# Kernel tuning notes

Hardware: AMD Instinct MI355X
Metric: run time of the kernel (lower is better)

The kernel has to match this reference:

```python
import jax, jax.numpy as jnp
from jax import lax
import numpy as np

D_MODEL = 1024
D_STATE = 64
D_CONV = 4
EXPAND = 2
HEADDIM = 64
D_INNER = EXPAND * D_MODEL          # 2048
NHEADS = D_INNER // HEADDIM         # 32
CHUNK = 64
CONV_DIM = D_INNER + 2 * D_STATE    # 2176
D_IN_PROJ = 2 * D_INNER + 2 * D_STATE + NHEADS  # 4256
B_SZ = 4
SEQLEN = 2048
EPS = 1e-5


def _silu(x):
    return x * jax.nn.sigmoid(x)


def _segsum(x):
    # x: [..., T]; returns [..., T, T] with [i,j] = sum_{j<k<=i} x[k], -inf above diag
    T = x.shape[-1]
    xe = jnp.broadcast_to(x[..., None], x.shape + (T,))
    strict_lower = jnp.tril(jnp.ones((T, T), bool), -1)
    xe = jnp.where(strict_lower, xe, 0.0)
    s = jnp.cumsum(xe, axis=-2)
    lower = jnp.tril(jnp.ones((T, T), bool), 0)
    return jnp.where(lower, s, -jnp.inf)


def setup_inputs() -> dict:
    key = jax.random.key(0)
    ks = jax.random.split(key, 5)
    u = jax.random.normal(ks[0], (B_SZ, SEQLEN, D_MODEL), jnp.float32)
    W_in = jax.random.normal(ks[1], (D_IN_PROJ, D_MODEL), jnp.float32) * 0.02
    conv_w = jax.random.normal(ks[2], (CONV_DIM, 1, D_CONV), jnp.float32) * 0.2  # depthwise kernel
    conv_b = jnp.zeros((CONV_DIM,), jnp.float32)
    dt_bias = jax.random.uniform(ks[3], (NHEADS,), jnp.float32, -1.0, 1.0)
    A_log = jnp.log(jnp.linspace(1.0, float(NHEADS), NHEADS)).astype(jnp.float32)
    D = jnp.ones((NHEADS,), jnp.float32)
    norm_w = jnp.ones((D_INNER,), jnp.float32)
    W_out = jax.random.normal(ks[4], (D_MODEL, D_INNER), jnp.float32) * 0.02
    return dict(u=u, W_in=W_in, conv_w=conv_w, conv_b=conv_b, dt_bias=dt_bias,
                A_log=A_log, D=D, norm_w=norm_w, W_out=W_out)


def reference(u, W_in, conv_w, conv_b, dt_bias, A_log, D, norm_w, W_out):
    b, s, _ = u.shape
    A = -jnp.exp(A_log)                                   # [H]
    zxbcdt = u @ W_in.T                                   # [b,s,D_IN_PROJ]
    z = zxbcdt[..., :D_INNER]
    xBC = zxbcdt[..., D_INNER:D_INNER + CONV_DIM]
    dt = jax.nn.softplus(zxbcdt[..., D_INNER + CONV_DIM:] + dt_bias)  # [b,s,H]

    # causal depthwise conv1d (left pad d_conv-1 == torch pad-both + slice[:s])
    xc = lax.conv_general_dilated(
        xBC.transpose(0, 2, 1), conv_w, window_strides=(1,),
        padding=[(D_CONV - 1, 0)], feature_group_count=CONV_DIM,
        dimension_numbers=('NCH', 'OIH', 'NCH'))
    xBC = _silu(xc.transpose(0, 2, 1) + conv_b)           # [b,s,CONV_DIM]

    x = xBC[..., :D_INNER].reshape(b, s, NHEADS, HEADDIM)
    Bm = xBC[..., D_INNER:D_INNER + D_STATE]              # [b,s,N]
    Cm = xBC[..., D_INNER + D_STATE:]                     # [b,s,N]

    # SSD chunked scan
    nch = s // CHUNK
    xs = (x * dt[..., None]).reshape(b, nch, CHUNK, NHEADS, HEADDIM)
    Ad = (A * dt).reshape(b, nch, CHUNK, NHEADS)
    Br = Bm.reshape(b, nch, CHUNK, D_STATE)
    Cr = Cm.reshape(b, nch, CHUNK, D_STATE)
    A_ch = Ad.transpose(0, 1, 3, 2)                       # [b,c,h,l]
    A_cum = jnp.cumsum(A_ch, axis=-1)
    L = jnp.exp(_segsum(A_ch))                            # [b,c,h,l,l]
    Y_diag = jnp.einsum('bcln,bcsn,bchls,bcshp->bclhp', Cr, Br, L, xs)
    decay_states = jnp.exp(A_cum[..., -1:] - A_cum)       # [b,c,h,l]
    states = jnp.einsum('bchl,bcln,bclhp->bchpn', decay_states, Br, xs)
    init = jnp.zeros((b, 1, NHEADS, HEADDIM, D_STATE), xs.dtype)
    states = jnp.concatenate([init, states], axis=1)      # [b,c+1,h,p,n]
    total_decay = jnp.pad(A_cum[..., -1].transpose(0, 2, 1), ((0, 0), (0, 0), (1, 0)))
    decay_chunk = jnp.exp(_segsum(total_decay))           # [b,h,c+1,c+1]
    new_states = jnp.einsum('bhzc,bchpn->bzhpn', decay_chunk, states)
    states = new_states[:, :-1]                           # [b,c,h,p,n]
    state_decay_out = jnp.exp(A_cum)
    Y_off = jnp.einsum('bcln,bchpn,bchl->bclhp', Cr, states, state_decay_out)
    y = (Y_diag + Y_off).reshape(b, s, NHEADS, HEADDIM)

    y = y + x * D[:, None]
    y = y.reshape(b, s, D_INNER)
    # gated RMSNorm
    y = y * _silu(z)
    y = y * lax.rsqrt(jnp.mean(y * y, axis=-1, keepdims=True) + EPS) * norm_w
    return y @ W_out.T
```

## Files before the change

### kernel.cpp

```cpp
#include <hip/hip_runtime.h>
#include <hip/hip_bf16.h>

#define BSZ 4
#define SEQ 2048
#define DMODEL 1024
#define DINNER 2048
#define DSTATE 64
#define NH 32
#define HD 64
#define CKL 64
#define NCH 32
#define CONVD 2176
#define DPROJ 4256
#define N1 4224
#define MTOT 8192
#define YSTR 72

typedef __hip_bfloat16 bf16;
typedef __attribute__((ext_vector_type(8))) short short8;
typedef __attribute__((ext_vector_type(4))) short short4_;
typedef __attribute__((ext_vector_type(4))) float f32x4;

__device__ __forceinline__ float sigmoidf_(float x) { return 1.0f / (1.0f + __expf(-x)); }
__device__ __forceinline__ float bits2f(short s) { return __uint_as_float(((unsigned)(unsigned short)s) << 16); }
__device__ __forceinline__ short f2bits(float f) {
    bf16 h = __float2bfloat16(f);
    return *reinterpret_cast<short*>(&h);
}

__device__ __forceinline__ void gl_lds16(const bf16* g, bf16* l) {
    __builtin_amdgcn_global_load_lds((const __attribute__((address_space(1))) void*)g,
                                     (__attribute__((address_space(3))) void*)l, 16, 0, 0);
}

__device__ __forceinline__ void swzx(int& bx, int& by) {
    int nx = gridDim.x;
    int nwg = nx * gridDim.y;
    int Lr = blockIdx.y * nx + blockIdx.x;
    int L = (Lr & 7) * (nwg >> 3) + (Lr >> 3);
    int GSZ = nx * 8;
    int g = L / GSZ, r = L - g * GSZ;
    bx = r % nx;
    by = g * 8 + r / nx;
}

__global__ void k_cvt2(const float* __restrict__ W_in, const float* __restrict__ W_out,
                       const float* __restrict__ nw, bf16* __restrict__ win_b,
                       bf16* __restrict__ wout_b) {
    int g = (blockIdx.x * 256 + threadIdx.x) * 4;
    if (g < N1 * DMODEL) {
        f32x4 f = *(const f32x4*)&W_in[g];
        short4_ o;
#pragma unroll
        for (int j = 0; j < 4; j++) o[j] = f2bits(f[j]);
        *(short4_*)&win_b[g] = o;
    } else if (g < N1 * DMODEL + DMODEL * DINNER) {
        int g2 = g - N1 * DMODEL;
        f32x4 f = *(const f32x4*)&W_out[g2];
        f32x4 w = *(const f32x4*)&nw[g2 & (DINNER - 1)];
        short4_ o;
#pragma unroll
        for (int j = 0; j < 4; j++) o[j] = f2bits(f[j] * w[j]);
        *(short4_*)&wout_b[g2] = o;
    }
}

__global__ __launch_bounds__(256) void k_gemm_bt(const bf16* __restrict__ A, const bf16* __restrict__ W,
                                                 bf16* __restrict__ C, int N, int K, int lda) {
    __shared__ __align__(16) bf16 lA[128 * 64];
    __shared__ __align__(16) bf16 lB[128 * 64];
    const int tid = threadIdx.x;
    const int lane = tid & 63, w = tid >> 6;
    const int wm = w >> 1, wn = w & 1;
    const int lr = lane & 15, lk = lane >> 4;
    int bx, by;
    swzx(bx, by);
    const int m0 = by * 128, n0 = bx * 128;

    f32x4 acc[4][4];
#pragma unroll
    for (int i = 0; i < 4; i++)
#pragma unroll
        for (int j = 0; j < 4; j++) acc[i][j] = (f32x4){0.f, 0.f, 0.f, 0.f};

    const int r = tid >> 3;
    const int cs = ((tid & 7) ^ (r & 7)) * 8;
    const bf16* ga = A + (size_t)(m0 + r) * lda + cs;
    const bf16* gb = W + (size_t)(n0 + r) * K + cs;
    bf16* la0 = lA + tid * 8;
    bf16* lb0 = lB + tid * 8;
    const int sx = (lr & 7);

    for (int kt = 0; kt < K; kt += 64) {
#pragma unroll
        for (int i = 0; i < 4; i++) {
            gl_lds16(ga + kt + (size_t)(32 * i) * lda, la0 + 2048 * i);
            gl_lds16(gb + kt + (size_t)(32 * i) * K, lb0 + 2048 * i);
        }
        __syncthreads();
#pragma unroll
        for (int hh = 0; hh < 2; hh++) {
            const int cb = ((lk + 4 * hh) ^ sx) * 8;
            short8 af[4], bfr[4];
#pragma unroll
            for (int im = 0; im < 4; im++)
                af[im] = *(const short8*)&lA[(wm * 64 + im * 16 + lr) * 64 + cb];
#pragma unroll
            for (int jn = 0; jn < 4; jn++)
                bfr[jn] = *(const short8*)&lB[(wn * 64 + jn * 16 + lr) * 64 + cb];
#pragma unroll
            for (int im = 0; im < 4; im++)
#pragma unroll
                for (int jn = 0; jn < 4; jn++)
                    acc[im][jn] = __builtin_amdgcn_mfma_f32_16x16x32_bf16(af[im], bfr[jn], acc[im][jn], 0, 0, 0);
        }
        __syncthreads();
    }
#pragma unroll
    for (int im = 0; im < 4; im++) {
        int row = m0 + wm * 64 + im * 16 + lk * 4;
#pragma unroll
        for (int jn = 0; jn < 4; jn++) {
            int col = n0 + wn * 64 + jn * 16 + lr;
            bf16* cp = C + (size_t)row * N + col;
#pragma unroll
            for (int rr = 0; rr < 4; rr++) cp[(size_t)rr * N] = __float2bfloat16(acc[im][jn][rr]);
        }
    }
}

__global__ __launch_bounds__(256) void k_gemm2(const bf16* __restrict__ A, const bf16* __restrict__ W,
                                               float* __restrict__ C) {
    __shared__ __align__(16) bf16 lA[128 * 64];
    __shared__ __align__(16) bf16 lB[128 * 64];
    __shared__ float rsrow[128];
    const int tid = threadIdx.x;
    const int lane = tid & 63, w = tid >> 6;
    const int wm = w >> 1, wn = w & 1;
    const int lr = lane & 15, lk = lane >> 4;
    int bx, by;
    swzx(bx, by);
    const int m0 = by * 128, n0 = bx * 128;
    const int K = DINNER, N = DMODEL;

    f32x4 acc[4][4];
#pragma unroll
    for (int i = 0; i < 4; i++)
#pragma unroll
        for (int j = 0; j < 4; j++) acc[i][j] = (f32x4){0.f, 0.f, 0.f, 0.f};
    float ssq[4] = {0.f, 0.f, 0.f, 0.f};

    const int r = tid >> 3;
    const int cs = ((tid & 7) ^ (r & 7)) * 8;
    const bf16* ga = A + (size_t)(m0 + r) * N1 + cs;
    const bf16* gb = W + (size_t)(n0 + r) * K + cs;
    bf16* la0 = lA + tid * 8;
    bf16* lb0 = lB + tid * 8;
    const int sx = (lr & 7);

    for (int kt = 0; kt < K; kt += 64) {
#pragma unroll
        for (int i = 0; i < 4; i++) {
            gl_lds16(ga + kt + (size_t)(32 * i) * N1, la0 + 2048 * i);
            gl_lds16(gb + kt + (size_t)(32 * i) * K, lb0 + 2048 * i);
        }
        __syncthreads();
#pragma unroll
        for (int hh = 0; hh < 2; hh++) {
            const int cb = ((lk + 4 * hh) ^ sx) * 8;
            short8 af[4], bfr[4];
#pragma unroll
            for (int im = 0; im < 4; im++) {
                af[im] = *(const short8*)&lA[(wm * 64 + im * 16 + lr) * 64 + cb];
#pragma unroll
                for (int j = 0; j < 8; j++) { float v = bits2f(af[im][j]); ssq[im] += v * v; }
            }
#pragma unroll
            for (int jn = 0; jn < 4; jn++)
                bfr[jn] = *(const short8*)&lB[(wn * 64 + jn * 16 + lr) * 64 + cb];
#pragma unroll
            for (int im = 0; im < 4; im++)
#pragma unroll
                for (int jn = 0; jn < 4; jn++)
                    acc[im][jn] = __builtin_amdgcn_mfma_f32_16x16x32_bf16(af[im], bfr[jn], acc[im][jn], 0, 0, 0);
        }
        __syncthreads();
    }
#pragma unroll
    for (int im = 0; im < 4; im++) {
        float s = ssq[im];
        s += __shfl_down(s, 32);
        s += __shfl_down(s, 16);
        if (lane < 16) rsrow[wm * 64 + im * 16 + lane] = rsqrtf(s * (1.0f / DINNER) + 1e-5f);
    }
    __syncthreads();
#pragma unroll
    for (int im = 0; im < 4; im++) {
        int rloc = wm * 64 + im * 16 + lk * 4;
        int row = m0 + rloc;
#pragma unroll
        for (int rr = 0; rr < 4; rr++) {
            float s = rsrow[rloc + rr];
#pragma unroll
            for (int jn = 0; jn < 4; jn++) {
                int col = n0 + wn * 64 + jn * 16 + lr;
                C[(size_t)(row + rr) * N + col] = acc[im][jn][rr] * s;
            }
        }
    }
}

__global__ __launch_bounds__(256) void k_prep(const float* __restrict__ u, const float* __restrict__ W_in,
                                              const float* __restrict__ dt_bias,
                                              bf16* __restrict__ u_b, float* __restrict__ dtt) {
    __shared__ __align__(16) float us[8 * DMODEL];
    const int t0 = blockIdx.x * 8;
    const int tid = threadIdx.x;
    const float* ur = u + (size_t)t0 * DMODEL;
    bf16* ub = u_b + (size_t)t0 * DMODEL;
#pragma unroll
    for (int i = 0; i < 8; i++) {
        int idx = (i * 256 + tid) * 4;
        f32x4 v = *(const f32x4*)&ur[idx];
        *(f32x4*)&us[idx] = v;
        short4_ o;
#pragma unroll
        for (int j = 0; j < 4; j++) o[j] = f2bits(v[j]);
        *(short4_*)&ub[idx] = o;
    }
    __syncthreads();
    const int h = tid >> 3, sub = tid & 7;
    const float* wr = W_in + (size_t)(DPROJ - NH + h) * DMODEL;
    float s[8] = {};
    for (int k = sub * 4; k < DMODEL; k += 32) {
        f32x4 w4 = *(const f32x4*)&wr[k];
#pragma unroll
        for (int rr = 0; rr < 8; rr++) {
            const float* up = &us[rr * DMODEL + k];
            s[rr] += up[0] * w4[0] + up[1] * w4[1] + up[2] * w4[2] + up[3] * w4[3];
        }
    }
#pragma unroll
    for (int rr = 0; rr < 8; rr++) {
        s[rr] += __shfl_down(s[rr], 4, 8);
        s[rr] += __shfl_down(s[rr], 2, 8);
        s[rr] += __shfl_down(s[rr], 1, 8);
    }
    if (sub == 0) {
        float bh = dt_bias[h];
#pragma unroll
        for (int rr = 0; rr < 8; rr++) {
            float x = s[rr] + bh;
            dtt[(size_t)h * MTOT + t0 + rr] = (x > 20.f) ? x : log1pf(__expf(x));
        }
    }
}

__global__ void k_conv(const bf16* __restrict__ zx, const float* __restrict__ cw,
                       const float* __restrict__ cb, bf16* __restrict__ xbc) {
    int g = (blockIdx.x * 256 + threadIdx.x) * 4;
    if (g >= MTOT * CONVD) return;
    int c0 = g % CONVD;
    int t = g / CONVD;
    int s = t & (SEQ - 1);
    const short* base = (const short*)(zx + (size_t)t * N1 + DINNER + c0);
    f32x4 w0 = *(const f32x4*)&cw[(c0 + 0) * 4];
    f32x4 w1 = *(const f32x4*)&cw[(c0 + 1) * 4];
    f32x4 w2 = *(const f32x4*)&cw[(c0 + 2) * 4];
    f32x4 w3 = *(const f32x4*)&cw[(c0 + 3) * 4];
    f32x4 a = *(const f32x4*)&cb[c0];
#pragma unroll
    for (int k = 0; k < 4; k++) {
        int st = s - 3 + k;
        if (st >= 0) {
            short4_ v = *(const short4_*)(base + (long)(k - 3) * N1);
            a[0] += bits2f(v[0]) * w0[k];
            a[1] += bits2f(v[1]) * w1[k];
            a[2] += bits2f(v[2]) * w2[k];
            a[3] += bits2f(v[3]) * w3[k];
        }
    }
    short4_ o;
#pragma unroll
    for (int j = 0; j < 4; j++) o[j] = f2bits(a[j] * sigmoidf_(a[j]));
    *(short4_*)&xbc[g] = o;
}

__global__ __launch_bounds__(256) void k_ssd(const bf16* __restrict__ xbc, const float* __restrict__ dtt,
                                             const float* __restrict__ A_log, const float* __restrict__ Dp,
                                             bf16* __restrict__ zx) {
    __shared__ __align__(16) short Ct[2][64 * YSTR];
    __shared__ __align__(16) short Bt[2][64 * YSTR];
    __shared__ __align__(16) short Bn[2][64 * YSTR];
    __shared__ __align__(16) short Xt[2][32 * YSTR];
    __shared__ __align__(16) short Sb[2][32 * YSTR];
    __shared__ __align__(16) short Gs[4 * 16 * YSTR];
    __shared__ __align__(16) float Sf[32 * 68];
    __shared__ __align__(16) float sdt2[2][64], sAc2[2][64], sf2[2][64];
    __shared__ float set2[2];

    const int ph = blockIdx.x, h = blockIdx.y, b = blockIdx.z;
    const int tid = threadIdx.x;
    const int lane = tid & 63, w = tid >> 6;
    const int lr = lane & 15, lk = lane >> 4;
    const float Ah = -__expf(A_log[h]);
    const float Dh = Dp[h];
    const int xcol = h * HD + ph * 32;

    const int lrow = tid >> 2, c0 = (tid & 3) * 16, px = (tid & 3) * 8;
    const int zl = 16 * w + (lane >> 2), zp = (lane & 3) * 8;

    short8 rC0, rC1, rB0, rB1, rX, rZ;
    float rdt;
    auto load_chunk = [&](int cc) {
        int rows0 = b * SEQ + cc * CKL;
        const short* rp = (const short*)(xbc + (size_t)(rows0 + lrow) * CONVD);
        rC0 = *(const short8*)&rp[DINNER + DSTATE + c0];
        rC1 = *(const short8*)&rp[DINNER + DSTATE + c0 + 8];
        rB0 = *(const short8*)&rp[DINNER + c0];
        rB1 = *(const short8*)&rp[DINNER + c0 + 8];
        rX  = *(const short8*)&rp[xcol + px];
        rZ  = *(const short8*)((const short*)zx + (size_t)(rows0 + zl) * N1 + xcol + zp);
        rdt = dtt[(size_t)h * MTOT + rows0 + lane];
    };
    auto scatter = [&](int buf) {
        *(short8*)&Ct[buf][lrow * YSTR + c0] = rC0;
        *(short8*)&Ct[buf][lrow * YSTR + c0 + 8] = rC1;
        *(short8*)&Bt[buf][lrow * YSTR + c0] = rB0;
        *(short8*)&Bt[buf][lrow * YSTR + c0 + 8] = rB1;
#pragma unroll
        for (int j = 0; j < 8; j++) {
            Bn[buf][(c0 + j) * YSTR + lrow] = rB0[j];
            Bn[buf][(c0 + 8 + j) * YSTR + lrow] = rB1[j];
            Xt[buf][(px + j) * YSTR + lrow] = rX[j];
        }
    };
    auto dtscan = [&](int buf) {
        if (tid < 64) {
            float dv = rdt;
            float v = Ah * dv;
#pragma unroll
            for (int d = 1; d < 64; d <<= 1) { float o = __shfl_up(v, d); if (tid >= d) v += o; }
            float tot = __shfl(v, 63);
            sdt2[buf][tid] = dv; sAc2[buf][tid] = v; sf2[buf][tid] = __expf(tot - v) * dv;
            if (tid == 63) set2[buf] = __expf(tot);
        }
    };

    for (int i = tid; i < 32 * 68; i += 256) Sf[i] = 0.f;
    for (int i = tid; i < 32 * YSTR; i += 256) Sb[0][i] = 0;
    load_chunk(0);
    scatter(0);
    dtscan(0);
    __syncthreads();

    for (int c = 0; c < NCH; c++) {
        const int par = c & 1, nb = par ^ 1;
        const int rows0 = b * SEQ + c * CKL;
        float etot = set2[par];
        short8 zcur = rZ;
        if (c + 1 < NCH) load_chunk(c + 1);

        short8 cf0 = *(const short8*)&Ct[par][(16 * w + lr) * YSTR + lk * 8];
        short8 cf1 = *(const short8*)&Ct[par][(16 * w + lr) * YSTR + 32 + lk * 8];
        f32x4 acc[2];
#pragma unroll
        for (int t = 0; t < 2; t++) {
            short8 s0 = *(const short8*)&Sb[par][(16 * t + lr) * YSTR + lk * 8];
            short8 s1 = *(const short8*)&Sb[par][(16 * t + lr) * YSTR + 32 + lk * 8];
            acc[t] = __builtin_amdgcn_mfma_f32_16x16x32_bf16(cf0, s0, (f32x4){0.f, 0.f, 0.f, 0.f}, 0, 0, 0);
            acc[t] = __builtin_amdgcn_mfma_f32_16x16x32_bf16(cf1, s1, acc[t], 0, 0, 0);
        }
        float sAcl[4], el[4];
#pragma unroll
        for (int rr = 0; rr < 4; rr++) { sAcl[rr] = sAc2[par][16 * w + lk * 4 + rr]; el[rr] = __expf(sAcl[rr]); }
#pragma unroll
        for (int t = 0; t < 2; t++)
#pragma unroll
            for (int rr = 0; rr < 4; rr++) acc[t][rr] *= el[rr];
        short* gw = Gs + w * 16 * YSTR;
#pragma unroll
        for (int t = 0; t < 4; t++) {
            short8 b0 = *(const short8*)&Bt[par][(16 * t + lr) * YSTR + lk * 8];
            short8 b1 = *(const short8*)&Bt[par][(16 * t + lr) * YSTR + 32 + lk * 8];
            f32x4 g = __builtin_amdgcn_mfma_f32_16x16x32_bf16(cf0, b0, (f32x4){0.f, 0.f, 0.f, 0.f}, 0, 0, 0);
            g = __builtin_amdgcn_mfma_f32_16x16x32_bf16(cf1, b1, g, 0, 0, 0);
            int s = 16 * t + lr;
            float sAcs = sAc2[par][s], dts = sdt2[par][s];
#pragma unroll
            for (int rr = 0; rr < 4; rr++) {
                int l = 16 * w + lk * 4 + rr;
                float v = (s <= l) ? g[rr] * __expf(sAcl[rr] - sAcs) * dts : 0.f;
                gw[(lk * 4 + rr) * YSTR + s] = f2bits(v);
            }
        }
        short8 gf0 = *(const short8*)&gw[lr * YSTR + lk * 8];
        short8 gf1 = *(const short8*)&gw[lr * YSTR + 32 + lk * 8];
#pragma unroll
        for (int t = 0; t < 2; t++) {
            short8 x0 = *(const short8*)&Xt[par][(16 * t + lr) * YSTR + lk * 8];
            short8 x1 = *(const short8*)&Xt[par][(16 * t + lr) * YSTR + 32 + lk * 8];
            acc[t] = __builtin_amdgcn_mfma_f32_16x16x32_bf16(gf0, x0, acc[t], 0, 0, 0);
            acc[t] = __builtin_amdgcn_mfma_f32_16x16x32_bf16(gf1, x1, acc[t], 0, 0, 0);
        }
        {
            int pw = w & 1, nh2 = w >> 1;
            short8 xt0 = *(const short8*)&Xt[par][(16 * pw + lr) * YSTR + lk * 8];
            short8 xt1 = *(const short8*)&Xt[par][(16 * pw + lr) * YSTR + 32 + lk * 8];
            f32x4 sa0 = *(const f32x4*)&sf2[par][lk * 8];
            f32x4 sa1 = *(const f32x4*)&sf2[par][lk * 8 + 4];
            f32x4 sb0 = *(const f32x4*)&sf2[par][32 + lk * 8];
            f32x4 sb1 = *(const f32x4*)&sf2[par][32 + lk * 8 + 4];
            short8 xd0, xd1;
#pragma unroll
            for (int j = 0; j < 4; j++) {
                xd0[j]     = f2bits(bits2f(xt0[j])     * sa0[j]);
                xd0[4 + j] = f2bits(bits2f(xt0[4 + j]) * sa1[j]);
                xd1[j]     = f2bits(bits2f(xt1[j])     * sb0[j]);
                xd1[4 + j] = f2bits(bits2f(xt1[4 + j]) * sb1[j]);
            }
#pragma unroll
            for (int j = 0; j < 2; j++) {
                int nt = 2 * nh2 + j;
                short8 b0 = *(const short8*)&Bn[par][(16 * nt + lr) * YSTR + lk * 8];
                short8 b1 = *(const short8*)&Bn[par][(16 * nt + lr) * YSTR + 32 + lk * 8];
                f32x4 sacc = __builtin_amdgcn_mfma_f32_16x16x32_bf16(xd0, b0, (f32x4){0.f, 0.f, 0.f, 0.f}, 0, 0, 0);
                sacc = __builtin_amdgcn_mfma_f32_16x16x32_bf16(xd1, b1, sacc, 0, 0, 0);
#pragma unroll
                for (int rr = 0; rr < 4; rr++) {
                    int n = 16 * nt + lr;
                    int p = 16 * pw + lk * 4 + rr;
                    float nv = Sf[p * 68 + n] * etot + sacc[rr];
                    Sf[p * 68 + n] = nv;
                    Sb[nb][p * YSTR + n] = f2bits(nv);
                }
            }
        }
#pragma unroll
        for (int t = 0; t < 2; t++) {
#pragma unroll
            for (int rr = 0; rr < 4; rr++) {
                int p = 16 * t + lr;
                int l = 16 * w + lk * 4 + rr;
                float y = acc[t][rr] + Dh * bits2f(Xt[par][p * YSTR + l]);
                Ct[par][l * YSTR + p] = f2bits(y);
            }
        }
        {
            short8 y8 = *(const short8*)&Ct[par][zl * YSTR + zp];
            short* zpp = (short*)zx + (size_t)(rows0 + zl) * N1 + xcol + zp;
            short8 o;
#pragma unroll
            for (int j = 0; j < 8; j++) {
                float z = bits2f(zcur[j]);
                o[j] = f2bits(bits2f(y8[j]) * (z * sigmoidf_(z)));
            }
            *(short8*)zpp = o;
        }
        if (c + 1 < NCH) {
            scatter(nb);
            dtscan(nb);
        }
        __syncthreads();
    }
}

extern "C" void kernel_launch(void* const* d_in, const int* in_sizes, int n_in,
                              void* d_out, int out_size, void* d_ws, size_t ws_size,
                              hipStream_t stream) {
    const float* u       = (const float*)d_in[0];
    const float* W_in    = (const float*)d_in[1];
    const float* conv_w  = (const float*)d_in[2];
    const float* conv_b  = (const float*)d_in[3];
    const float* dt_bias = (const float*)d_in[4];
    const float* A_log   = (const float*)d_in[5];
    const float* Dp      = (const float*)d_in[6];
    const float* norm_w  = (const float*)d_in[7];
    const float* W_out   = (const float*)d_in[8];
    float* out = (float*)d_out;

    char* ws = (char*)d_ws;
    bf16* zx     = (bf16*)ws;  ws += (size_t)MTOT * N1 * 2;
    bf16* xbc    = (bf16*)ws;  ws += (size_t)MTOT * CONVD * 2;
    bf16* wout_b = (bf16*)ws;  ws += (size_t)DMODEL * DINNER * 2;
    float* dtt   = (float*)ws; ws += (size_t)NH * MTOT * 4;

    bf16* u_b   = (bf16*)d_out;
    bf16* win_b = (bf16*)((char*)d_out + (size_t)MTOT * DMODEL * 2);

    k_prep<<<MTOT / 8, 256, 0, stream>>>(u, W_in, dt_bias, u_b, dtt);
    k_cvt2<<<((N1 * DMODEL + DMODEL * DINNER) / 4 + 255) / 256, 256, 0, stream>>>(
        W_in, W_out, norm_w, win_b, wout_b);

    k_gemm_bt<<<dim3(N1 / 128, MTOT / 128), 256, 0, stream>>>(u_b, win_b, zx, N1, DMODEL, DMODEL);

    k_conv<<<(MTOT * CONVD / 4 + 255) / 256, 256, 0, stream>>>(zx, conv_w, conv_b, xbc);

    k_ssd<<<dim3(2, NH, BSZ), 256, 0, stream>>>(xbc, dtt, A_log, Dp, zx);

    k_gemm2<<<dim3(DMODEL / 128, MTOT / 128), 256, 0, stream>>>(zx, wout_b, out);
}
```

Measured before the change: 393.8 us.

## Rewrite both GEMMs with larger tiles and software-pipelined LDS buffering

Replaces the two 128x128 single-buffered GEMM kernels with 512-thread kernels on larger tiles: 256x192 for the input projection and 256x128 for the output projection. The new kernels double- or triple-buffer LDS and issue global-to-LDS prefetches for later k-tiles while MFMAs run on the current one. They use explicit vmcnt waits, barriers and s_setprio phases to hide memory latency and remove the stall-heavy sync-load-sync loop. In exchange LDS use and register pressure rise, fewer workgroups are launched, and the hand-counted waitcnt scheduling is fragile.

```diff
diff --git a/kernel.cpp b/kernel.cpp
--- a/kernel.cpp
+++ b/kernel.cpp
@@ -33,6 +33,17 @@
                                      (__attribute__((address_space(3))) void*)l, 16, 0, 0);
 }
 
+__device__ __forceinline__ f32x4 MF(short8 a, short8 b, f32x4 c) {
+    return __builtin_amdgcn_mfma_f32_16x16x32_bf16(a, b, c, 0, 0, 0);
+}
+
+template<int N> __device__ __forceinline__ void vmw() {
+    if constexpr (N == 0)      asm volatile("s_waitcnt vmcnt(0)" ::: "memory");
+    else if constexpr (N == 3) asm volatile("s_waitcnt vmcnt(3)" ::: "memory");
+    else if constexpr (N == 6) asm volatile("s_waitcnt vmcnt(6)" ::: "memory");
+    else                       asm volatile("s_waitcnt vmcnt(15)" ::: "memory");
+}
+
 __device__ __forceinline__ void swzx(int& bx, int& by) {
     int nx = gridDim.x;
     int nwg = nx * gridDim.y;
@@ -65,83 +76,167 @@
     }
 }
 
-__global__ __launch_bounds__(256) void k_gemm_bt(const bf16* __restrict__ A, const bf16* __restrict__ W,
-                                                 bf16* __restrict__ C, int N, int K, int lda) {
-    __shared__ __align__(16) bf16 lA[128 * 64];
-    __shared__ __align__(16) bf16 lB[128 * 64];
+#define BARWAIT()                                           \
+    __builtin_amdgcn_s_barrier();                           \
+    asm volatile("s_waitcnt lgkmcnt(0)" ::: "memory");      \
+    __builtin_amdgcn_sched_barrier(0);                      \
+    __builtin_amdgcn_s_setprio(1)
+#define ENDPH()                                             \
+    __builtin_amdgcn_s_setprio(0);                          \
+    __builtin_amdgcn_s_barrier()
+
+__global__ __launch_bounds__(512, 2) void k_g1(const bf16* __restrict__ Ap,
+                                               const bf16* __restrict__ Wp,
+                                               bf16* __restrict__ Cp) {
+    __shared__ __align__(16) short sA[2][16384];
+    __shared__ __align__(16) short sB[2][12288];
+    const int tid = threadIdx.x;
+    const int lane = tid & 63, w = tid >> 6;
+    const int wm = w >> 2, wn = w & 3;
+    const int lr = lane & 15, lk = lane >> 4;
+    int bx, by; swzx(bx, by);
+    const int m0 = by * 256, n0 = bx * 192;
+    const int ld = DMODEL;
+
+    const int r8 = tid >> 3;
+    const int c8 = ((tid & 7) ^ (r8 & 7)) * 8;
+    const bf16* pA = Ap + (size_t)(m0 + r8) * ld + c8;
+    const bf16* pB = Wp + (size_t)(n0 + r8) * ld + c8;
+
+    auto stA = [&](int d, int t) {
+#pragma unroll
+        for (int h = 0; h < 2; h++)
+#pragma unroll
+            for (int q = 0; q < 2; q++)
+                gl_lds16(pA + (size_t)(h * 128 + q * 64) * ld + t * 64,
+                         (bf16*)&sA[d][h * 8192 + q * 4096 + tid * 8]);
+    };
+    auto stB = [&](int d, int u, int t) {
+        gl_lds16(pB + (size_t)(u * 64) * ld + t * 64,
+                 (bf16*)&sB[d][u * 4096 + tid * 8]);
+    };
+
+    const int c0 = (lk ^ (lr & 7)) * 8;
+    const int c1 = ((lk + 4) ^ (lr & 7)) * 8;
+    const int aR = (wm * 128 + lr) * 64;
+    const int bR = (wn * 48 + lr) * 64;
+
+    f32x4 acc[8][3];
+#pragma unroll
+    for (int i = 0; i < 8; i++)
+#pragma unroll
+        for (int j = 0; j < 3; j++) acc[i][j] = (f32x4){0.f, 0.f, 0.f, 0.f};
+    short8 bfr[3][2], af[2][2];
+
+#define RDA1(D, I)                                                   \
+    af[0][0] = *(const short8*)&sA[D][aR + (I) * 1024 + c0];         \
+    af[0][1] = *(const short8*)&sA[D][aR + (I) * 1024 + c1];         \
+    af[1][0] = *(const short8*)&sA[D][aR + (I + 1) * 1024 + c0];     \
+    af[1][1] = *(const short8*)&sA[D][aR + (I + 1) * 1024 + c1]
+#define RDB1(D)                                                      \
+    _Pragma("unroll")                                                \
+    for (int jn = 0; jn < 3; ++jn) {                                 \
+        bfr[jn][0] = *(const short8*)&sB[D][bR + jn * 1024 + c0];    \
+        bfr[jn][1] = *(const short8*)&sB[D][bR + jn * 1024 + c1];    \
+    }
+#define MM1(I)                                                       \
+    _Pragma("unroll")                                                \
+    for (int hh = 0; hh < 2; ++hh) {                                 \
+        _Pragma("unroll")                                            \
+        for (int jn = 0; jn < 3; ++jn) {                             \
+            acc[I][jn]     = MF(af[0][hh], bfr[jn][hh], acc[I][jn]); \
+            acc[I + 1][jn] = MF(af[1][hh], bfr[jn][hh], acc[I + 1][jn]); \
+        }                                                            \
+    }
+
+    stB(0, 0, 0); stB(0, 1, 0); stB(0, 2, 0); stA(0, 0);
+    stB(1, 0, 1); stB(1, 1, 1); stB(1, 2, 1);
+    vmw<3>();
+    __builtin_amdgcn_s_barrier();
+
+    for (int t0 = 0; t0 < 16; t0 += 2) {
+        const int t1 = t0 + 1, t2 = t0 + 2, t3 = t0 + 3;
+        const bool more = (t2 < 16);
+        RDB1(0); RDA1(0, 0);
+        stA(1, t1);
+        BARWAIT(); MM1(0); ENDPH();
+        RDA1(0, 2); if (more) stB(0, 0, t2);
+        BARWAIT(); MM1(2); ENDPH();
+        RDA1(0, 4); if (more) stB(0, 1, t2);
+        BARWAIT(); MM1(4); ENDPH();
+        RDA1(0, 6); if (more) stB(0, 2, t2);
+        BARWAIT(); MM1(6);
+        __builtin_amdgcn_s_setprio(0);
+        if (more) vmw<3>(); else vmw<0>();
+        __builtin_amdgcn_s_barrier();
+        RDB1(1); RDA1(1, 0);
+        if (more) stA(0, t2);
+        BARWAIT(); MM1(0); ENDPH();
+        RDA1(1, 2); if (more) stB(1, 0, t3);
+        BARWAIT(); MM1(2); ENDPH();
+        RDA1(1, 4); if (more) stB(1, 1, t3);
+        BARWAIT(); MM1(4); ENDPH();
+        RDA1(1, 6); if (more) stB(1, 2, t3);
+        BARWAIT(); MM1(6);
+        __builtin_amdgcn_s_setprio(0);
+        if (more) vmw<3>();
+        __builtin_amdgcn_s_barrier();
+    }
+#undef RDA1
+#undef RDB1
+#undef MM1
+
+#pragma unroll
+    for (int im = 0; im < 8; im++) {
+        int row = m0 + wm * 128 + im * 16 + lk * 4;
+#pragma unroll
+        for (int jn = 0; jn < 3; jn++) {
+            int col = n0 + wn * 48 + jn * 16 + lr;
+            bf16* cp = Cp + (size_t)row * N1 + col;
+#pragma unroll
+            for (int rr = 0; rr < 4; rr++) cp[(size_t)rr * N1] = __float2bfloat16(acc[im][jn][rr]);
+        }
+    }
+}
+
+__global__ __launch_bounds__(512, 2) void k_g2(const bf16* __restrict__ Ap,
+                                               const bf16* __restrict__ Wp,
+                                               float* __restrict__ Cp) {
+    __shared__ __align__(16) short sA[3][16384];
+    __shared__ __align__(16) short sB[3][8192];
+    __shared__ float rsrow[256];
     const int tid = threadIdx.x;
     const int lane = tid & 63, w = tid >> 6;
     const int wm = w >> 1, wn = w & 1;
     const int lr = lane & 15, lk = lane >> 4;
-    int bx, by;
-    swzx(bx, by);
-    const int m0 = by * 128, n0 = bx * 128;
-
-    f32x4 acc[4][4];
-#pragma unroll
-    for (int i = 0; i < 4; i++)
-#pragma unroll
-        for (int j = 0; j < 4; j++) acc[i][j] = (f32x4){0.f, 0.f, 0.f, 0.f};
-
-    const int r = tid >> 3;
-    const int cs = ((tid & 7) ^ (r & 7)) * 8;
-    const bf16* ga = A + (size_t)(m0 + r) * lda + cs;
-    const bf16* gb = W + (size_t)(n0 + r) * K + cs;
-    bf16* la0 = lA + tid * 8;
-    bf16* lb0 = lB + tid * 8;
-    const int sx = (lr & 7);
-
-    for (int kt = 0; kt < K; kt += 64) {
-#pragma unroll
-        for (int i = 0; i < 4; i++) {
-            gl_lds16(ga + kt + (size_t)(32 * i) * lda, la0 + 2048 * i);
-            gl_lds16(gb + kt + (size_t)(32 * i) * K, lb0 + 2048 * i);
-        }
-        __syncthreads();
-#pragma unroll
-        for (int hh = 0; hh < 2; hh++) {
-            const int cb = ((lk + 4 * hh) ^ sx) * 8;
-            short8 af[4], bfr[4];
-#pragma unroll
-            for (int im = 0; im < 4; im++)
-                af[im] = *(const short8*)&lA[(wm * 64 + im * 16 + lr) * 64 + cb];
-#pragma unroll
-            for (int jn = 0; jn < 4; jn++)
-                bfr[jn] = *(const short8*)&lB[(wn * 64 + jn * 16 + lr) * 64 + cb];
-#pragma unroll
-            for (int im = 0; im < 4; im++)
-#pragma unroll
-                for (int jn = 0; jn < 4; jn++)
-                    acc[im][jn] = __builtin_amdgcn_mfma_f32_16x16x32_bf16(af[im], bfr[jn], acc[im][jn], 0, 0, 0);
-        }
-        __syncthreads();
-    }
-#pragma unroll
-    for (int im = 0; im < 4; im++) {
-        int row = m0 + wm * 64 + im * 16 + lk * 4;
-#pragma unroll
-        for (int jn = 0; jn < 4; jn++) {
-            int col = n0 + wn * 64 + jn * 16 + lr;
-            bf16* cp = C + (size_t)row * N + col;
-#pragma unroll
-            for (int rr = 0; rr < 4; rr++) cp[(size_t)rr * N] = __float2bfloat16(acc[im][jn][rr]);
-        }
-    }
-}
-
-__global__ __launch_bounds__(256) void k_gemm2(const bf16* __restrict__ A, const bf16* __restrict__ W,
-                                               float* __restrict__ C) {
-    __shared__ __align__(16) bf16 lA[128 * 64];
-    __shared__ __align__(16) bf16 lB[128 * 64];
-    __shared__ float rsrow[128];
-    const int tid = threadIdx.x;
-    const int lane = tid & 63, w = tid >> 6;
-    const int wm = w >> 1, wn = w & 1;
-    const int lr = lane & 15, lk = lane >> 4;
-    int bx, by;
-    swzx(bx, by);
-    const int m0 = by * 128, n0 = bx * 128;
-    const int K = DINNER, N = DMODEL;
+    int bx, by; swzx(bx, by);
+    const int m0 = by * 256, n0 = bx * 128;
+    const int lda = N1, ldb = DINNER;
+
+    const int r8 = tid >> 3;
+    const int c8 = ((tid & 7) ^ (r8 & 7)) * 8;
+    const bf16* pA = Ap + (size_t)(m0 + r8) * lda + c8;
+    const bf16* pB = Wp + (size_t)(n0 + r8) * ldb + c8;
+
+    auto stA = [&](int d, int t) {
+#pragma unroll
+        for (int h = 0; h < 2; h++)
+#pragma unroll
+            for (int q = 0; q < 2; q++)
+                gl_lds16(pA + (size_t)(h * 128 + q * 64) * lda + t * 64,
+                         (bf16*)&sA[d][h * 8192 + q * 4096 + tid * 8]);
+    };
+    auto stB = [&](int d, int t) {
+#pragma unroll
+        for (int q = 0; q < 2; q++)
+            gl_lds16(pB + (size_t)(q * 64) * ldb + t * 64,
+                     (bf16*)&sB[d][q * 4096 + tid * 8]);
+    };
+
+    const int c0 = (lk ^ (lr & 7)) * 8;
+    const int c1 = ((lk + 4) ^ (lr & 7)) * 8;
+    const int aR = (wm * 64 + lr) * 64;
+    const int bR = (wn * 64 + lr) * 64;
 
     f32x4 acc[4][4];
 #pragma unroll
@@ -149,43 +244,62 @@
 #pragma unroll
         for (int j = 0; j < 4; j++) acc[i][j] = (f32x4){0.f, 0.f, 0.f, 0.f};
     float ssq[4] = {0.f, 0.f, 0.f, 0.f};
-
-    const int r = tid >> 3;
-    const int cs = ((tid & 7) ^ (r & 7)) * 8;
-    const bf16* ga = A + (size_t)(m0 + r) * N1 + cs;
-    const bf16* gb = W + (size_t)(n0 + r) * K + cs;
-    bf16* la0 = lA + tid * 8;
-    bf16* lb0 = lB + tid * 8;
-    const int sx = (lr & 7);
-
-    for (int kt = 0; kt < K; kt += 64) {
-#pragma unroll
-        for (int i = 0; i < 4; i++) {
-            gl_lds16(ga + kt + (size_t)(32 * i) * N1, la0 + 2048 * i);
-            gl_lds16(gb + kt + (size_t)(32 * i) * K, lb0 + 2048 * i);
-        }
-        __syncthreads();
-#pragma unroll
-        for (int hh = 0; hh < 2; hh++) {
-            const int cb = ((lk + 4 * hh) ^ sx) * 8;
-            short8 af[4], bfr[4];
-#pragma unroll
-            for (int im = 0; im < 4; im++) {
-                af[im] = *(const short8*)&lA[(wm * 64 + im * 16 + lr) * 64 + cb];
-#pragma unroll
-                for (int j = 0; j < 8; j++) { float v = bits2f(af[im][j]); ssq[im] += v * v; }
-            }
-#pragma unroll
-            for (int jn = 0; jn < 4; jn++)
-                bfr[jn] = *(const short8*)&lB[(wn * 64 + jn * 16 + lr) * 64 + cb];
-#pragma unroll
-            for (int im = 0; im < 4; im++)
-#pragma unroll
-                for (int jn = 0; jn < 4; jn++)
-                    acc[im][jn] = __builtin_amdgcn_mfma_f32_16x16x32_bf16(af[im], bfr[jn], acc[im][jn], 0, 0, 0);
-        }
-        __syncthreads();
-    }
+    short8 bfr[4][2], af[2][2];
+
+#define RDA2(D, I)                                                   \
+    af[0][0] = *(const short8*)&sA[D][aR + (I) * 1024 + c0];         \
+    af[0][1] = *(const short8*)&sA[D][aR + (I) * 1024 + c1];         \
+    af[1][0] = *(const short8*)&sA[D][aR + (I + 1) * 1024 + c0];     \
+    af[1][1] = *(const short8*)&sA[D][aR + (I + 1) * 1024 + c1]
+#define RDB2(D)                                                      \
+    _Pragma("unroll")                                                \
+    for (int jn = 0; jn < 4; ++jn) {                                 \
+        bfr[jn][0] = *(const short8*)&sB[D][bR + jn * 1024 + c0];    \
+        bfr[jn][1] = *(const short8*)&sB[D][bR + jn * 1024 + c1];    \
+    }
+#define MM2(I)                                                       \
+    _Pragma("unroll")                                                \
+    for (int hh = 0; hh < 2; ++hh) {                                 \
+        _Pragma("unroll")                                            \
+        for (int jn = 0; jn < 4; ++jn) {                             \
+            acc[I][jn]     = MF(af[0][hh], bfr[jn][hh], acc[I][jn]); \
+            acc[I + 1][jn] = MF(af[1][hh], bfr[jn][hh], acc[I + 1][jn]); \
+        }                                                            \
+    }
+#define SSQ2(I)                                                      \
+    _Pragma("unroll")                                                \
+    for (int hh = 0; hh < 2; ++hh)                                   \
+        _Pragma("unroll")                                            \
+        for (int e = 0; e < 8; ++e) {                                \
+            float v0 = bits2f(af[0][hh][e]), v1 = bits2f(af[1][hh][e]); \
+            ssq[I] += v0 * v0; ssq[I + 1] += v1 * v1;                \
+        }
+
+    stB(0, 0); stA(0, 0);
+    stB(1, 1); stA(1, 1);
+    vmw<6>();
+    __builtin_amdgcn_s_barrier();
+
+    int rb = 0, sb = 2;
+    for (int t = 0; t < 32; ++t) {
+        const bool more = (t + 2 < 32);
+        RDB2(rb); RDA2(rb, 0);
+        if (more) stB(sb, t + 2);
+        BARWAIT(); MM2(0); SSQ2(0); ENDPH();
+        RDA2(rb, 2);
+        if (more) stA(sb, t + 2);
+        BARWAIT(); MM2(2); SSQ2(2);
+        __builtin_amdgcn_s_setprio(0);
+        if (more) vmw<6>(); else if (t + 1 < 32) vmw<0>();
+        __builtin_amdgcn_s_barrier();
+        rb = (rb == 2) ? 0 : rb + 1;
+        sb = (sb == 2) ? 0 : sb + 1;
+    }
+#undef RDA2
+#undef RDB2
+#undef MM2
+#undef SSQ2
+
 #pragma unroll
     for (int im = 0; im < 4; im++) {
         float s = ssq[im];
@@ -196,15 +310,15 @@
     __syncthreads();
 #pragma unroll
     for (int im = 0; im < 4; im++) {
-        int rloc = wm * 64 + im * 16 + lk * 4;
-        int row = m0 + rloc;
+        int rl = wm * 64 + im * 16 + lk * 4;
+        int row = m0 + rl;
 #pragma unroll
         for (int rr = 0; rr < 4; rr++) {
-            float s = rsrow[rloc + rr];
+            float s = rsrow[rl + rr];
 #pragma unroll
             for (int jn = 0; jn < 4; jn++) {
                 int col = n0 + wn * 64 + jn * 16 + lr;
-                C[(size_t)(row + rr) * N + col] = acc[im][jn][rr] * s;
+                Cp[(size_t)(row + rr) * DMODEL + col] = acc[im][jn][rr] * s;
             }
         }
     }
@@ -492,11 +606,11 @@
     k_cvt2<<<((N1 * DMODEL + DMODEL * DINNER) / 4 + 255) / 256, 256, 0, stream>>>(
         W_in, W_out, norm_w, win_b, wout_b);
 
-    k_gemm_bt<<<dim3(N1 / 128, MTOT / 128), 256, 0, stream>>>(u_b, win_b, zx, N1, DMODEL, DMODEL);
+    k_g1<<<dim3(N1 / 192, MTOT / 256), 512, 0, stream>>>(u_b, win_b, zx);
 
     k_conv<<<(MTOT * CONVD / 4 + 255) / 256, 256, 0, stream>>>(zx, conv_w, conv_b, xbc);
 
     k_ssd<<<dim3(2, NH, BSZ), 256, 0, stream>>>(xbc, dtt, A_log, Dp, zx);
 
-    k_gemm2<<<dim3(DMODEL / 128, MTOT / 128), 256, 0, stream>>>(zx, wout_b, out);
-}
+    k_g2<<<dim3(DMODEL / 128, MTOT / 256), 512, 0, stream>>>(zx, wout_b, out);
+}
```

Result: no change. 390.8 us (-0.8%).
